# Optimization experiments

Measured on AMD Instinct MI355X. Metric: run time of the kernel, lower is better.

The kernel has to match this reference:

```python
import jax, jax.numpy as jnp
import numpy as np

N_NODES = 100000
N_EDGES = 1250000
D_FEAT = 64


def setup_inputs() -> dict:
    key = jax.random.key(0)
    k1, k2 = jax.random.split(key)
    x = jax.random.normal(k1, (N_NODES, D_FEAT), dtype=jnp.float32)
    edge_index = jax.random.randint(k2, (2, N_EDGES), 0, N_NODES, dtype=jnp.int64)
    return {"t": 0, "x": x, "edge_index": edge_index}


def reference(t, x, edge_index):
    # LGConv(normalize=False): out[i] = sum_{(j->i) in E} x[j]
    # adj_t SpMM expressed as gather + segment-sum scatter.
    src = edge_index[0]  # source/neighbor nodes
    dst = edge_index[1]  # destination nodes
    msgs = x[src]  # [E, D] gather
    out = jax.ops.segment_sum(msgs, dst, num_segments=N_NODES)  # [N, D]
    return out
```

## Files before the change

### kernel.cpp

```cpp
#include <hip/hip_runtime.h>

#define N_NODES 100000
#define N_EDGES 1250000
#define D_FEAT 64

#define NB_SHIFT 7
#define NODES_PER_B 128
#define N_BUCKETS ((N_NODES + NODES_PER_B - 1) / NODES_PER_B)
#define TROW (N_BUCKETS + 1)
#define NB_PAD 1024
#define MAX_BUCKET_EDGES 2048
#define SRC_BITS 17
#define SRC_MASK ((1u << SRC_BITS) - 1u)

#define CH 8192
#define NCH ((N_EDGES + CH - 1) / CH)

__global__ __launch_bounds__(256) void lgconv_scatter(
    const float* __restrict__ x, const int* __restrict__ src,
    const int* __restrict__ dst, float* __restrict__ out) {
    int tid  = blockIdx.x * blockDim.x + threadIdx.x;
    int edge = tid >> 4;
    int f4   = (tid & 15) << 2;
    if (edge >= N_EDGES) return;
    int s = src[edge], d = dst[edge];
    const float4 v = *reinterpret_cast<const float4*>(x + (size_t)s * D_FEAT + f4);
    float* o = out + (size_t)d * D_FEAT + f4;
    unsafeAtomicAdd(o + 0, v.x); unsafeAtomicAdd(o + 1, v.y);
    unsafeAtomicAdd(o + 2, v.z); unsafeAtomicAdd(o + 3, v.w);
}

__device__ __forceinline__ unsigned short f2bf(float f) {
    unsigned int u = __float_as_uint(f);
    return (unsigned short)((u + 0x7FFFu + ((u >> 16) & 1u)) >> 16);
}
__device__ __forceinline__ float bflo(unsigned int p) {
    return __uint_as_float(p << 16);
}
__device__ __forceinline__ float bfhi(unsigned int p) {
    return __uint_as_float(p & 0xFFFF0000u);
}

__global__ __launch_bounds__(256) void conv_bf16(
    const float* __restrict__ x, unsigned short* __restrict__ xb) {
    const int F4 = N_NODES * D_FEAT / 4;
    int i = blockIdx.x * 256 + threadIdx.x;
    if (i >= F4) return;
    float4 v = reinterpret_cast<const float4*>(x)[i];
    ushort4 o;
    o.x = f2bf(v.x); o.y = f2bf(v.y); o.z = f2bf(v.z); o.w = f2bf(v.w);
    reinterpret_cast<ushort4*>(xb)[i] = o;
}

__global__ __launch_bounds__(1024) void k1_sort(
    const int* __restrict__ src, const int* __restrict__ dst,
    unsigned int* __restrict__ bins, int* __restrict__ table) {
    __shared__ int hist[NB_PAD];
    __shared__ int scanBase[NB_PAD];
    __shared__ int cur[NB_PAD];
    __shared__ int scanTmp[1024];
    __shared__ unsigned int stage[CH];
    const int t    = threadIdx.x;
    const int c    = blockIdx.x;
    const int base = c * CH;
    const int cnt  = min(CH, N_EDGES - base);
    hist[t] = 0; cur[t] = 0;
    __syncthreads();
    for (int i = t; i < cnt; i += 1024)
        atomicAdd(&hist[dst[base + i] >> NB_SHIFT], 1);
    __syncthreads();
    int v = hist[t];
    scanTmp[t] = v;
    __syncthreads();
    for (int off = 1; off < 1024; off <<= 1) {
        int u = (t >= off) ? scanTmp[t - off] : 0;
        __syncthreads();
        scanTmp[t] += u;
        __syncthreads();
    }
    scanBase[t] = scanTmp[t] - v;
    __syncthreads();
    if (t < TROW) table[c * TROW + t] = scanBase[t];
    for (int i = t; i < cnt; i += 1024) {
        int d = dst[base + i], s = src[base + i];
        int b = d >> NB_SHIFT;
        unsigned int packed = ((unsigned int)(d & (NODES_PER_B - 1)) << SRC_BITS)
                            | (unsigned int)s;
        int pos = scanBase[b] + atomicAdd(&cur[b], 1);
        stage[pos] = packed;
    }
    __syncthreads();
    for (int i = t; i < cnt; i += 1024) bins[base + i] = stage[i];
}

template <bool BF>
__global__ __launch_bounds__(512) void k2_accum(
    const float* __restrict__ x, const unsigned short* __restrict__ xb,
    const unsigned int* __restrict__ bins, const int* __restrict__ table,
    float* __restrict__ out) {
    __shared__ int            startA[512];
    __shared__ unsigned short lenA[512];
    __shared__ int            destB[512];
    __shared__ int            scanTmp[512];
    __shared__ unsigned int   raw[MAX_BUCKET_EDGES];
    __shared__ unsigned int   srcs[MAX_BUCKET_EDGES];
    __shared__ int cntArr[NODES_PER_B];
    __shared__ int nodeOff[NODES_PER_B + 1];
    __shared__ int curN[NODES_PER_B];
    __shared__ int s2[NODES_PER_B];
    const int t = threadIdx.x;
    const int b = blockIdx.x;

    int st = 0, len = 0;
    if (t < NCH) {
        st  = table[t * TROW + b];
        len = table[t * TROW + b + 1] - st;
    }
    startA[t] = st;
    lenA[t]   = (unsigned short)len;
    scanTmp[t] = len;
    __syncthreads();
    for (int off = 1; off < 512; off <<= 1) {
        int u = (t >= off) ? scanTmp[t - off] : 0;
        __syncthreads();
        scanTmp[t] += u;
        __syncthreads();
    }
    destB[t] = scanTmp[t] - len;
    int cntTot = scanTmp[511];
    if (cntTot > MAX_BUCKET_EDGES) cntTot = MAX_BUCKET_EDGES;
    if (t < NODES_PER_B) cntArr[t] = 0;
    __syncthreads();

    {
        const int cj = t >> 4;
        const int jj = t & 15;
        for (int c0 = 0; c0 < NCH; c0 += 32) {
            int c = c0 + cj;
            if (c < NCH) {
                int l = lenA[c], s0 = startA[c], db = destB[c];
                const unsigned int* p = bins + (size_t)c * CH + s0;
                if (jj < l) raw[db + jj] = p[jj];
                if (jj == 15)
                    for (int q = 16; q < l; ++q) raw[db + q] = p[q];
            }
        }
    }
    __syncthreads();

    for (int i = t; i < cntTot; i += 512)
        atomicAdd(&cntArr[raw[i] >> SRC_BITS], 1);
    __syncthreads();
    int v = (t < NODES_PER_B) ? cntArr[t] : 0;
    if (t < NODES_PER_B) s2[t] = v;
    __syncthreads();
    for (int off = 1; off < NODES_PER_B; off <<= 1) {
        int u = (t < NODES_PER_B && t >= off) ? s2[t - off] : 0;
        __syncthreads();
        if (t < NODES_PER_B) s2[t] += u;
        __syncthreads();
    }
    if (t < NODES_PER_B) { nodeOff[t] = s2[t] - v; curN[t] = s2[t] - v; }
    if (t == 0) nodeOff[NODES_PER_B] = cntTot;
    __syncthreads();
    for (int i = t; i < cntTot; i += 512) {
        unsigned int p = raw[i];
        int pos = atomicAdd(&curN[p >> SRC_BITS], 1);
        srcs[pos] = p & SRC_MASK;
    }
    __syncthreads();

    if (BF) {
        int f0 = (t & 7) << 3;
        for (int g = 0; g < NODES_PER_B / 64; ++g) {
            int local = g * 64 + (t >> 3);
            int node  = b * NODES_PER_B + local;
            int beg = nodeOff[local], end = nodeOff[local + 1];
            float a0=0,a1=0,a2=0,a3=0,a4=0,a5=0,a6=0,a7=0;
            int k = beg;
            for (; k + 1 < end; k += 2) {
                const uint4 u = *reinterpret_cast<const uint4*>(
                    xb + (size_t)srcs[k] * D_FEAT + f0);
                const uint4 w = *reinterpret_cast<const uint4*>(
                    xb + (size_t)srcs[k + 1] * D_FEAT + f0);
                a0 += bflo(u.x) + bflo(w.x); a1 += bfhi(u.x) + bfhi(w.x);
                a2 += bflo(u.y) + bflo(w.y); a3 += bfhi(u.y) + bfhi(w.y);
                a4 += bflo(u.z) + bflo(w.z); a5 += bfhi(u.z) + bfhi(w.z);
                a6 += bflo(u.w) + bflo(w.w); a7 += bfhi(u.w) + bfhi(w.w);
            }
            if (k < end) {
                const uint4 u = *reinterpret_cast<const uint4*>(
                    xb + (size_t)srcs[k] * D_FEAT + f0);
                a0 += bflo(u.x); a1 += bfhi(u.x);
                a2 += bflo(u.y); a3 += bfhi(u.y);
                a4 += bflo(u.z); a5 += bfhi(u.z);
                a6 += bflo(u.w); a7 += bfhi(u.w);
            }
            if (node < N_NODES) {
                float* op = out + (size_t)node * D_FEAT + f0;
                *reinterpret_cast<float4*>(op)     = make_float4(a0, a1, a2, a3);
                *reinterpret_cast<float4*>(op + 4) = make_float4(a4, a5, a6, a7);
            }
        }
    } else {
        int lane4 = (t & 15) << 2;
        for (int g = 0; g < NODES_PER_B / 32; ++g) {
            int local = g * 32 + (t >> 4);
            int node  = b * NODES_PER_B + local;
            int beg = nodeOff[local], end = nodeOff[local + 1];
            float4 acc = make_float4(0.f, 0.f, 0.f, 0.f);
            int k = beg;
            for (; k + 1 < end; k += 2) {
                unsigned int i0 = srcs[k], i1 = srcs[k + 1];
                const float4 a = *reinterpret_cast<const float4*>(x + (size_t)i0 * D_FEAT + lane4);
                const float4 c = *reinterpret_cast<const float4*>(x + (size_t)i1 * D_FEAT + lane4);
                acc.x += a.x + c.x; acc.y += a.y + c.y;
                acc.z += a.z + c.z; acc.w += a.w + c.w;
            }
            if (k < end) {
                unsigned int i0 = srcs[k];
                const float4 a = *reinterpret_cast<const float4*>(x + (size_t)i0 * D_FEAT + lane4);
                acc.x += a.x; acc.y += a.y; acc.z += a.z; acc.w += a.w;
            }
            if (node < N_NODES)
                *reinterpret_cast<float4*>(out + (size_t)node * D_FEAT + lane4) = acc;
        }
    }
}

extern "C" void kernel_launch(void* const* d_in, const int* in_sizes, int n_in,
                              void* d_out, int out_size, void* d_ws, size_t ws_size,
                              hipStream_t stream) {
    const float* x   = (const float*)d_in[1];
    const int*   ei  = (const int*)d_in[2];
    const int*   src = ei;
    const int*   dst = ei + N_EDGES;
    float*       out = (float*)d_out;

    const size_t tabBytes = (size_t)NCH * TROW * sizeof(int);
    const size_t binBytes = (size_t)N_EDGES * sizeof(unsigned int);
    const size_t xbOff    = (binBytes + tabBytes + 15) & ~(size_t)15;
    const size_t needA    = xbOff + (size_t)N_NODES * D_FEAT * sizeof(unsigned short);
    const size_t needB    = binBytes + tabBytes;

    if (ws_size >= needA) {
        unsigned int*   bins  = (unsigned int*)d_ws;
        int*            table = (int*)((char*)d_ws + binBytes);
        unsigned short* xb    = (unsigned short*)((char*)d_ws + xbOff);
        const int F4 = N_NODES * D_FEAT / 4;
        conv_bf16<<<(F4 + 255) / 256, 256, 0, stream>>>(x, xb);
        k1_sort<<<NCH, 1024, 0, stream>>>(src, dst, bins, table);
        k2_accum<true><<<N_BUCKETS, 512, 0, stream>>>(x, xb, bins, table, out);
    } else if (ws_size >= needB) {
        unsigned int* bins  = (unsigned int*)d_ws;
        int*          table = (int*)((char*)d_ws + binBytes);
        k1_sort<<<NCH, 1024, 0, stream>>>(src, dst, bins, table);
        k2_accum<false><<<N_BUCKETS, 512, 0, stream>>>(x, nullptr, bins, table, out);
    } else {
        hipMemsetAsync(out, 0, (size_t)out_size * sizeof(float), stream);
        const int total = N_EDGES * 16;
        lgconv_scatter<<<(total + 255) / 256, 256, 0, stream>>>(x, src, dst, out);
    }
}
```

Before: 141.3 us.

## Fuse bf16 conversion into sort kernel and wave-parallelize per-node gather

```diff
diff --git a/kernel.cpp b/kernel.cpp
--- a/kernel.cpp
+++ b/kernel.cpp
@@ -41,18 +41,9 @@
     return __uint_as_float(p & 0xFFFF0000u);
 }
 
-__global__ __launch_bounds__(256) void conv_bf16(
-    const float* __restrict__ x, unsigned short* __restrict__ xb) {
-    const int F4 = N_NODES * D_FEAT / 4;
-    int i = blockIdx.x * 256 + threadIdx.x;
-    if (i >= F4) return;
-    float4 v = reinterpret_cast<const float4*>(x)[i];
-    ushort4 o;
-    o.x = f2bf(v.x); o.y = f2bf(v.y); o.z = f2bf(v.z); o.w = f2bf(v.w);
-    reinterpret_cast<ushort4*>(xb)[i] = o;
-}
-
+template <bool CONV>
 __global__ __launch_bounds__(1024) void k1_sort(
+    const float* __restrict__ x, unsigned short* __restrict__ xb,
     const int* __restrict__ src, const int* __restrict__ dst,
     unsigned int* __restrict__ bins, int* __restrict__ table) {
     __shared__ int hist[NB_PAD];
@@ -64,6 +55,17 @@
     const int c    = blockIdx.x;
     const int base = c * CH;
     const int cnt  = min(CH, N_EDGES - base);
+
+    if (CONV) {
+        const int F4 = N_NODES * D_FEAT / 4;
+        for (int i = c * 1024 + t; i < F4; i += NCH * 1024) {
+            float4 v = reinterpret_cast<const float4*>(x)[i];
+            ushort4 o;
+            o.x = f2bf(v.x); o.y = f2bf(v.y); o.z = f2bf(v.z); o.w = f2bf(v.w);
+            reinterpret_cast<ushort4*>(xb)[i] = o;
+        }
+    }
+
     hist[t] = 0; cur[t] = 0;
     __syncthreads();
     for (int i = t; i < cnt; i += 1024)
@@ -171,24 +173,14 @@
     __syncthreads();
 
     if (BF) {
-        int f0 = (t & 7) << 3;
-        for (int g = 0; g < NODES_PER_B / 64; ++g) {
-            int local = g * 64 + (t >> 3);
-            int node  = b * NODES_PER_B + local;
+        const int wave = t >> 6;
+        const int lane = t & 63;
+        const int slot = lane >> 3;
+        const int f0   = (lane & 7) << 3;
+        for (int local = wave; local < NODES_PER_B; local += 8) {
             int beg = nodeOff[local], end = nodeOff[local + 1];
             float a0=0,a1=0,a2=0,a3=0,a4=0,a5=0,a6=0,a7=0;
-            int k = beg;
-            for (; k + 1 < end; k += 2) {
-                const uint4 u = *reinterpret_cast<const uint4*>(
-                    xb + (size_t)srcs[k] * D_FEAT + f0);
-                const uint4 w = *reinterpret_cast<const uint4*>(
-                    xb + (size_t)srcs[k + 1] * D_FEAT + f0);
-                a0 += bflo(u.x) + bflo(w.x); a1 += bfhi(u.x) + bfhi(w.x);
-                a2 += bflo(u.y) + bflo(w.y); a3 += bfhi(u.y) + bfhi(w.y);
-                a4 += bflo(u.z) + bflo(w.z); a5 += bfhi(u.z) + bfhi(w.z);
-                a6 += bflo(u.w) + bflo(w.w); a7 += bfhi(u.w) + bfhi(w.w);
-            }
-            if (k < end) {
+            for (int k = beg + slot; k < end; k += 8) {
                 const uint4 u = *reinterpret_cast<const uint4*>(
                     xb + (size_t)srcs[k] * D_FEAT + f0);
                 a0 += bflo(u.x); a1 += bfhi(u.x);
@@ -196,7 +188,15 @@
                 a4 += bflo(u.z); a5 += bfhi(u.z);
                 a6 += bflo(u.w); a7 += bfhi(u.w);
             }
-            if (node < N_NODES) {
+            #pragma unroll
+            for (int m = 8; m < 64; m <<= 1) {
+                a0 += __shfl_xor(a0, m, 64); a1 += __shfl_xor(a1, m, 64);
+                a2 += __shfl_xor(a2, m, 64); a3 += __shfl_xor(a3, m, 64);
+                a4 += __shfl_xor(a4, m, 64); a5 += __shfl_xor(a5, m, 64);
+                a6 += __shfl_xor(a6, m, 64); a7 += __shfl_xor(a7, m, 64);
+            }
+            int node = b * NODES_PER_B + local;
+            if (slot == 0 && node < N_NODES) {
                 float* op = out + (size_t)node * D_FEAT + f0;
                 *reinterpret_cast<float4*>(op)     = make_float4(a0, a1, a2, a3);
                 *reinterpret_cast<float4*>(op + 4) = make_float4(a4, a5, a6, a7);
@@ -247,14 +247,12 @@
         unsigned int*   bins  = (unsigned int*)d_ws;
         int*            table = (int*)((char*)d_ws + binBytes);
         unsigned short* xb    = (unsigned short*)((char*)d_ws + xbOff);
-        const int F4 = N_NODES * D_FEAT / 4;
-        conv_bf16<<<(F4 + 255) / 256, 256, 0, stream>>>(x, xb);
-        k1_sort<<<NCH, 1024, 0, stream>>>(src, dst, bins, table);
+        k1_sort<true><<<NCH, 1024, 0, stream>>>(x, xb, src, dst, bins, table);
         k2_accum<true><<<N_BUCKETS, 512, 0, stream>>>(x, xb, bins, table, out);
     } else if (ws_size >= needB) {
         unsigned int* bins  = (unsigned int*)d_ws;
         int*          table = (int*)((char*)d_ws + binBytes);
-        k1_sort<<<NCH, 1024, 0, stream>>>(src, dst, bins, table);
+        k1_sort<false><<<NCH, 1024, 0, stream>>>(x, nullptr, src, dst, bins, table);
         k2_accum<false><<<N_BUCKETS, 512, 0, stream>>>(x, nullptr, bins, table, out);
     } else {
         hipMemsetAsync(out, 0, (size_t)out_size * sizeof(float), stream);
```

New measurement: 142.9 us. Within noise of the previous version (+1.1%).
